# Performance work log

Measured on AMD Instinct MI355X. Metric: run time of the kernel, lower is better.

The kernel has to match this reference:

```python
import jax, jax.numpy as jnp
import numpy as np

K = 8               # top-k frequencies
PRED_LEN = 96       # prediction_length
LOW_FREQ = 1        # low_frequency cutoff (drops DC)


def setup_inputs() -> dict:
    key = jax.random.key(0)
    x = jax.random.normal(key, (32, 2048, 64), dtype=jnp.float32)
    return {"x": x}


def reference(x):
    b, t, d = x.shape
    x_freq = jnp.fft.rfft(x, axis=1)                 # (b, t//2+1, d) complex
    freqs = jnp.fft.rfftfreq(t).astype(x.dtype)
    if t % 2 == 0:
        x_freq = x_freq[:, LOW_FREQ:-1]              # drop DC and Nyquist
        f = freqs[LOW_FREQ:-1]
    else:
        x_freq = x_freq[:, LOW_FREQ:]
        f = freqs[LOW_FREQ:]

    # top-k over frequency dim (axis=1), independently per (b, d)
    mag = jnp.abs(x_freq)                            # (b, F, d)
    _, idx = jax.lax.top_k(jnp.moveaxis(mag, 1, 2), K)  # (b, d, K), sorted desc
    idx = jnp.moveaxis(idx, 1, 2)                    # (b, K, d)
    x_k = jnp.take_along_axis(x_freq, idx, axis=1)   # (b, K, d) complex
    f_k = f[idx]                                     # (b, K, d)

    # extrapolate: add conjugate (negative) frequencies, then cos-sum
    x2 = jnp.concatenate([x_k, jnp.conj(x_k)], axis=1)  # (b, 2K, d)
    f2 = jnp.concatenate([f_k, -f_k], axis=1)           # (b, 2K, d)
    t_val = jnp.arange(t + PRED_LEN, dtype=x.dtype)     # (T,)
    amp = jnp.abs(x2) / t                               # (b, 2K, d)
    phase = jnp.angle(x2)                               # (b, 2K, d)
    # (b, 2K, T, d) broadcast intermediate, reduced over freq axis
    x_time = amp[:, :, None, :] * jnp.cos(
        2.0 * np.float32(np.pi) * f2[:, :, None, :] * t_val[None, None, :, None]
        + phase[:, :, None, :]
    )
    return x_time.sum(axis=1)                        # (b, t+PRED_LEN, d)
```

## Files before the change

### kernel.cpp

```cpp
#include <hip/hip_runtime.h>
#include <math.h>

#define BB 32
#define TT 2048
#define DD 64
#define PRED 96
#define TP (TT + PRED)
#define KTOP 8
#define MARGIN 8e-4f
#define PI_D 3.14159265358979323846

__device__ __forceinline__ int br6(int l) { return (int)(__brev((unsigned)l) >> 26); }
static constexpr int BR5[32] = {0,16,8,24,4,20,12,28,2,18,10,26,6,22,14,30,
                                1,17,9,25,5,21,13,29,3,19,11,27,7,23,15,31};
static constexpr float C32T[16] = {
    1.0f, 0.98078528040323044913f, 0.92387953251128675613f, 0.83146961230254523708f,
    0.70710678118654752440f, 0.55557023301960222474f, 0.38268343236508977173f, 0.19509032201612826785f,
    0.0f, -0.19509032201612826785f, -0.38268343236508977173f, -0.55557023301960222474f,
    -0.70710678118654752440f, -0.83146961230254523708f, -0.92387953251128675613f, -0.98078528040323044913f};
static constexpr float S32T[16] = {
    0.0f, 0.19509032201612826785f, 0.38268343236508977173f, 0.55557023301960222474f,
    0.70710678118654752440f, 0.83146961230254523708f, 0.92387953251128675613f, 0.98078528040323044913f,
    1.0f, 0.98078528040323044913f, 0.92387953251128675613f, 0.83146961230254523708f,
    0.70710678118654752440f, 0.55557023301960222474f, 0.38268343236508977173f, 0.19509032201612826785f};

__device__ __forceinline__ float2 ctw(float2 a, int m) {
    const float rev = (float)m * (1.0f / 2048.0f);
    const float c = __builtin_amdgcn_cosf(rev);
    const float s = __builtin_amdgcn_sinf(rev);
    return make_float2(a.x * c + a.y * s, a.y * c - a.x * s);
}

__global__ __launch_bounds__(256) void fused_kernel(const float* __restrict__ x,
                                                    float* __restrict__ out) {
    __shared__ float SRe[4][2112];
    __shared__ float SIm[4][2112];
    __shared__ int   coefK[8][KTOP];
    __shared__ float coefR[8][KTOP], coefI[8][KTOP];

    const int t    = threadIdx.x;
    const int wv   = t >> 6, lane = t & 63;
    const int bid  = blockIdx.x;
    const int xcd  = bid & 7;
    const int idx  = bid >> 3;
    const int b    = xcd * 4 + (idx >> 3);
    const int grp  = idx & 7;
    const int dp   = grp * 4 + wv;
    const int d_base = grp * 8;

    const float2* xv = (const float2*)x;
    const size_t xbase = (size_t)b * TT * (DD / 2) + dp;

    float2 v[32];
    #pragma unroll
    for (int i = 0; i < 32; ++i)
        v[i] = xv[xbase + (size_t)(64 * BR5[i] + lane) * (DD / 2)];

    #pragma unroll
    for (int s = 1; s <= 5; ++s) {
        const int m = 1 << s, half = m >> 1, stepw = 32 >> s;
        #pragma unroll
        for (int g = 0; g < 32; g += m) {
            #pragma unroll
            for (int j = 0; j < half; ++j) {
                const float c = C32T[j * stepw], sn = S32T[j * stepw];
                const int i0 = g + j, i1 = i0 + half;
                const float tr = c * v[i1].x + sn * v[i1].y;
                const float ti = c * v[i1].y - sn * v[i1].x;
                v[i1] = make_float2(v[i0].x - tr, v[i0].y - ti);
                v[i0] = make_float2(v[i0].x + tr, v[i0].y + ti);
            }
        }
    }

    #pragma unroll
    for (int q = 1; q < 32; ++q) v[q] = ctw(v[q], (lane * q) & (TT - 1));

    {
        const int rl = br6(lane);
        #pragma unroll
        for (int q = 0; q < 32; ++q) {
            v[q].x = __shfl(v[q].x, rl, 64);
            v[q].y = __shfl(v[q].y, rl, 64);
        }
    }
    #pragma unroll
    for (int s = 1; s <= 6; ++s) {
        const int half = 1 << (s - 1);
        const float rev = (float)(lane & (half - 1)) / (float)(1 << s);
        const float wc  = __builtin_amdgcn_cosf(rev);
        const float wsn = __builtin_amdgcn_sinf(rev);
        const bool  hi  = (lane & half) != 0;
        #pragma unroll
        for (int q = 0; q < 32; ++q) {
            float2 pv;
            pv.x = __shfl_xor(v[q].x, half, 64);
            pv.y = __shfl_xor(v[q].y, half, 64);
            const float2 bsv = hi ? v[q] : pv;
            const float2 asv = hi ? pv : v[q];
            const float tr = wc * bsv.x + wsn * bsv.y;
            const float ti = wc * bsv.y - wsn * bsv.x;
            v[q] = hi ? make_float2(asv.x - tr, asv.y - ti)
                      : make_float2(asv.x + tr, asv.y + ti);
        }
    }

    #pragma unroll
    for (int q = 0; q < 32; ++q) {
        const int a = 33 * lane + q;
        SRe[wv][a] = v[q].x;
        SIm[wv][a] = v[q].y;
    }
    __syncthreads();

    const int sig = lane >> 5, hl = lane & 31;
    unsigned A[32];
    #pragma unroll
    for (int q = 0; q < 32; ++q) {
        const int k = 32 * hl + q;
        unsigned kk = 0u;
        if (k != 0) {
            const int a1 = k + (k >> 5);
            const int pk = TT - k, a2 = pk + (pk >> 5);
            const float zr = SRe[wv][a1], zi = SIm[wv][a1];
            const float yr = SRe[wv][a2], yi = SIm[wv][a2];
            float cr, ci;
            if (sig == 0) { cr = 0.5f * (zr + yr); ci = 0.5f * (zi - yi); }
            else          { cr = 0.5f * (zi + yi); ci = 0.5f * (yr - zr); }
            const float mg = cr * cr + ci * ci;
            kk = (__float_as_uint(mg) & 0xFFFFF800u) | (unsigned)(2047 - k);
        }
        A[q] = kk;
    }

    #pragma unroll
    for (int sz = 2; sz <= 32; sz <<= 1) {
        #pragma unroll
        for (int d = sz >> 1; d > 0; d >>= 1) {
            #pragma unroll
            for (int i2 = 0; i2 < 32; ++i2) {
                const int j2i = i2 ^ d;
                if (j2i > i2) {
                    const bool desc = ((i2 & sz) == 0);
                    const unsigned a = A[i2], b2 = A[j2i];
                    const unsigned mx = a > b2 ? a : b2, mn = a > b2 ? b2 : a;
                    A[i2] = desc ? mx : mn;  A[j2i] = desc ? mn : mx;
                }
            }
        }
    }
    #pragma unroll
    for (int off = 1; off <= 16; off <<= 1) {
        unsigned Bv[32];
        #pragma unroll
        for (int i2 = 0; i2 < 32; ++i2)
            Bv[i2] = (unsigned)__shfl_xor((int)A[i2], off, 64);
        #pragma unroll
        for (int i2 = 0; i2 < 32; ++i2) {
            const unsigned o = Bv[31 - i2];
            A[i2] = A[i2] > o ? A[i2] : o;
        }
        #pragma unroll
        for (int d = 16; d > 0; d >>= 1) {
            #pragma unroll
            for (int i2 = 0; i2 < 32; ++i2) {
                if ((i2 & d) == 0) {
                    const int j2i = i2 + d;
                    const unsigned a = A[i2], b2 = A[j2i];
                    A[i2] = a > b2 ? a : b2;  A[j2i] = a > b2 ? b2 : a;
                }
            }
        }
    }

    const float m8f = __uint_as_float(A[7] & 0xFFFFF800u);
    unsigned bandmask = 0u;
    #pragma unroll
    for (int r = 0; r < 16; ++r) {
        const float mr = __uint_as_float(A[r] & 0xFFFFF800u);
        if (fabsf(mr - m8f) <= MARGIN * m8f) bandmask |= (1u << r);
    }
    const int flg = (bandmask != (1u << 7)) ? 1 : 0;

    unsigned myk = 0u;
    #pragma unroll
    for (int i2 = 0; i2 < 16; ++i2) myk = (hl == i2) ? A[i2] : myk;
    const int kcand = 2047 - (int)(myk & 0x7FFu);
    const int s_local = 2 * wv + sig;

    if (!flg && hl < KTOP) {
        const int k = kcand, a1 = k + (k >> 5), pk = TT - k, a2 = pk + (pk >> 5);
        const float zr = SRe[wv][a1], zi = SIm[wv][a1];
        const float yr = SRe[wv][a2], yi = SIm[wv][a2];
        float cr, ci;
        if (sig == 0) { cr = 0.5f * (zr + yr); ci = 0.5f * (zi - yi); }
        else          { cr = 0.5f * (zi + yi); ci = 0.5f * (yr - zr); }
        coefK[s_local][hl] = k;
        coefR[s_local][hl] = cr * (2.0f / (float)TT);
        coefI[s_local][hl] = ci * (2.0f / (float)TT);
    }

    const int flg0 = __shfl(flg, 0, 64);
    const int flg1 = __shfl(flg, 32, 64);

    if (flg0 | flg1) {
        float2 sv[32];
        #pragma unroll
        for (int m = 0; m < 32; ++m)
            sv[m] = xv[xbase + (size_t)(lane + 64 * m) * (DD / 2)];
        const double thA = -2.0 * PI_D * (double)lane / 64.0;
        const double thB = -2.0 * PI_D * (double)lane / (double)TT;
        const double wac = cos(thA), was = sin(thA);
        const double wbc = cos(thB), wbs = sin(thB);

        for (int sg = 0; sg < 2; ++sg) {
            const int flg_s = (sg == 0) ? flg0 : flg1;
            if (!flg_s) continue;
            const unsigned bm = (unsigned)__shfl((int)bandmask, 32 * sg, 64);
            const int lo = (int)__builtin_ctz(bm);
            double myM = 0.0, myR = 0.0, myI = 0.0;
            for (int r = 0; r < 16; ++r) {
                if (!((bm >> r) & 1u)) continue;
                const int kr = __shfl(kcand, 32 * sg + r, 64);
                double ar = 0.0, ai = 0.0;
                for (int m = 0; m < 32; ++m) {
                    const int n  = lane + 64 * m;
                    const int mm = (n * kr) & (TT - 1);
                    const double qc  = __shfl(wac, mm >> 5, 64);
                    const double qs  = __shfl(was, mm >> 5, 64);
                    const double rc2 = __shfl(wbc, mm & 31, 64);
                    const double rs2 = __shfl(wbs, mm & 31, 64);
                    const double wr = qc * rc2 - qs * rs2;
                    const double wi = qc * rs2 + qs * rc2;
                    const double xs = (sg == 0) ? (double)sv[m].x : (double)sv[m].y;
                    ar = fma(xs, wr, ar);
                    ai = fma(xs, wi, ai);
                }
                #pragma unroll
                for (int off = 32; off; off >>= 1) {
                    ar += __shfl_xor(ar, off, 64);
                    ai += __shfl_xor(ai, off, 64);
                }
                if (lane == 32 * sg + r) { myM = ar * ar + ai * ai; myR = ar; myI = ai; }
            }
            const int h16 = hl & 15;
            const double selfM = __shfl(myM, 32 * sg + h16, 64);
            const int    selfK = __shfl(kcand, 32 * sg + h16, 64);
            int rb = 0;
            for (int r2 = 0; r2 < 16; ++r2) {
                if (!((bm >> r2) & 1u)) continue;
                const double om = __shfl(myM, 32 * sg + r2, 64);
                const int    ok = __shfl(kcand, 32 * sg + r2, 64);
                if (r2 != h16 && (om > selfM || (om == selfM && ok < selfK))) ++rb;
            }
            const int isband = (int)((bm >> h16) & 1u);
            const int rank = isband ? (lo + rb) : h16;
            if (sig == sg && hl < 16 && rank < KTOP) {
                coefK[s_local][rank] = kcand;
                if (isband) {
                    coefR[s_local][rank] = (float)(myR * (2.0 / (double)TT));
                    coefI[s_local][rank] = (float)(myI * (2.0 / (double)TT));
                } else {
                    const int k = kcand, a1 = k + (k >> 5), pk = TT - k, a2 = pk + (pk >> 5);
                    const float zr = SRe[wv][a1], zi = SIm[wv][a1];
                    const float yr = SRe[wv][a2], yi = SIm[wv][a2];
                    float cr, ci;
                    if (sg == 0) { cr = 0.5f * (zr + yr); ci = 0.5f * (zi - yi); }
                    else          { cr = 0.5f * (zi + yi); ci = 0.5f * (yr - zr); }
                    coefR[s_local][rank] = cr * (2.0f / (float)TT);
                    coefI[s_local][rank] = ci * (2.0f / (float)TT);
                }
            }
        }
    }
    __syncthreads();

    const int d8 = t & 7, tq = t >> 3;
    int   kc[KTOP];
    float fr[KTOP], fi[KTOP], pc[KTOP], ps[KTOP], rc[KTOP], rs[KTOP];
    #pragma unroll
    for (int p = 0; p < KTOP; ++p) {
        kc[p] = coefK[d8][p];
        fr[p] = coefR[d8][p];
        fi[p] = coefI[d8][p];
        const int j0 = (kc[p] * tq) & (TT - 1);
        const float rv0 = (float)j0 * (1.0f / 2048.0f);
        pc[p] = __builtin_amdgcn_cosf(rv0);
        ps[p] = __builtin_amdgcn_sinf(rv0);
        const int jr = (kc[p] * 32) & (TT - 1);
        const float rvr = (float)jr * (1.0f / 2048.0f);
        rc[p] = __builtin_amdgcn_cosf(rvr);
        rs[p] = __builtin_amdgcn_sinf(rvr);
    }
    float* op = out + (size_t)b * TP * DD + d_base + d8;
    #pragma unroll 4
    for (int m = 0; m < 67; ++m) {
        const int tv = tq + 32 * m;
        float acc = 0.0f;
        #pragma unroll
        for (int p = 0; p < KTOP; ++p) acc += fr[p] * pc[p] - fi[p] * ps[p];
        op[(size_t)tv * DD] = acc;
        #pragma unroll
        for (int p = 0; p < KTOP; ++p) {
            const float nc = pc[p] * rc[p] - ps[p] * rs[p];
            const float ns = pc[p] * rs[p] + ps[p] * rc[p];
            pc[p] = nc; ps[p] = ns;
        }
    }
}

extern "C" void kernel_launch(void* const* d_in, const int* in_sizes, int n_in,
                              void* d_out, int out_size, void* d_ws, size_t ws_size,
                              hipStream_t stream) {
    const float* x = (const float*)d_in[0];
    float* out = (float*)d_out;
    (void)d_ws; (void)ws_size; (void)in_sizes; (void)n_in; (void)out_size;

    fused_kernel<<<BB * 8, 256, 0, stream>>>(x, out);
}
```

Measured before the change: 112.6 us.

## Stage output through reused LDS pool, trim top-k merge, drop redundant barrier

Merges the FFT scratch arrays into one shared pool. After the coefficient barrier, that pool is reused as an output tile, and the tile is written back to global memory in a flat thread-indexed loop. The cross-lane top-k merge now keeps only the top 16 candidates instead of 32, which cuts shuffles and compare-swaps. The barrier after the per-wave FFT store is removed because each wave reads only its own slice. The staged write still emits 8-float row segments at stride 64, much like before, so it adds LDS traffic and a barrier for little coalescing gain.

```diff
diff --git a/kernel.cpp b/kernel.cpp
--- a/kernel.cpp
+++ b/kernel.cpp
@@ -31,10 +31,13 @@
     return make_float2(a.x * c + a.y * s, a.y * c - a.x * s);
 }
 
+#define SRE(w,a) POOL[(w) * 2112 + (a)]
+#define SIM(w,a) POOL[8448 + (w) * 2112 + (a)]
+#define TILE(tv,d8) POOL[(tv) * 8 + (d8)]
+
 __global__ __launch_bounds__(256) void fused_kernel(const float* __restrict__ x,
                                                     float* __restrict__ out) {
-    __shared__ float SRe[4][2112];
-    __shared__ float SIm[4][2112];
+    __shared__ float POOL[17152];
     __shared__ int   coefK[8][KTOP];
     __shared__ float coefR[8][KTOP], coefI[8][KTOP];
 
@@ -108,10 +111,9 @@
     #pragma unroll
     for (int q = 0; q < 32; ++q) {
         const int a = 33 * lane + q;
-        SRe[wv][a] = v[q].x;
-        SIm[wv][a] = v[q].y;
-    }
-    __syncthreads();
+        SRE(wv, a) = v[q].x;
+        SIM(wv, a) = v[q].y;
+    }
 
     const int sig = lane >> 5, hl = lane & 31;
     unsigned A[32];
@@ -122,8 +124,8 @@
         if (k != 0) {
             const int a1 = k + (k >> 5);
             const int pk = TT - k, a2 = pk + (pk >> 5);
-            const float zr = SRe[wv][a1], zi = SIm[wv][a1];
-            const float yr = SRe[wv][a2], yi = SIm[wv][a2];
+            const float zr = SRE(wv, a1), zi = SIM(wv, a1);
+            const float yr = SRE(wv, a2), yi = SIM(wv, a2);
             float cr, ci;
             if (sig == 0) { cr = 0.5f * (zr + yr); ci = 0.5f * (zi - yi); }
             else          { cr = 0.5f * (zi + yi); ci = 0.5f * (yr - zr); }
@@ -151,19 +153,19 @@
     }
     #pragma unroll
     for (int off = 1; off <= 16; off <<= 1) {
-        unsigned Bv[32];
-        #pragma unroll
-        for (int i2 = 0; i2 < 32; ++i2)
+        unsigned Bv[16];
+        #pragma unroll
+        for (int i2 = 0; i2 < 16; ++i2)
             Bv[i2] = (unsigned)__shfl_xor((int)A[i2], off, 64);
         #pragma unroll
-        for (int i2 = 0; i2 < 32; ++i2) {
-            const unsigned o = Bv[31 - i2];
+        for (int i2 = 0; i2 < 16; ++i2) {
+            const unsigned o = Bv[15 - i2];
             A[i2] = A[i2] > o ? A[i2] : o;
         }
         #pragma unroll
-        for (int d = 16; d > 0; d >>= 1) {
+        for (int d = 8; d > 0; d >>= 1) {
             #pragma unroll
-            for (int i2 = 0; i2 < 32; ++i2) {
+            for (int i2 = 0; i2 < 16; ++i2) {
                 if ((i2 & d) == 0) {
                     const int j2i = i2 + d;
                     const unsigned a = A[i2], b2 = A[j2i];
@@ -190,8 +192,8 @@
 
     if (!flg && hl < KTOP) {
         const int k = kcand, a1 = k + (k >> 5), pk = TT - k, a2 = pk + (pk >> 5);
-        const float zr = SRe[wv][a1], zi = SIm[wv][a1];
-        const float yr = SRe[wv][a2], yi = SIm[wv][a2];
+        const float zr = SRE(wv, a1), zi = SIM(wv, a1);
+        const float yr = SRE(wv, a2), yi = SIM(wv, a2);
         float cr, ci;
         if (sig == 0) { cr = 0.5f * (zr + yr); ci = 0.5f * (zi - yi); }
         else          { cr = 0.5f * (zi + yi); ci = 0.5f * (yr - zr); }
@@ -262,8 +264,8 @@
                     coefI[s_local][rank] = (float)(myI * (2.0 / (double)TT));
                 } else {
                     const int k = kcand, a1 = k + (k >> 5), pk = TT - k, a2 = pk + (pk >> 5);
-                    const float zr = SRe[wv][a1], zi = SIm[wv][a1];
-                    const float yr = SRe[wv][a2], yi = SIm[wv][a2];
+                    const float zr = SRE(wv, a1), zi = SIM(wv, a1);
+                    const float yr = SRE(wv, a2), yi = SIM(wv, a2);
                     float cr, ci;
                     if (sg == 0) { cr = 0.5f * (zr + yr); ci = 0.5f * (zi - yi); }
                     else          { cr = 0.5f * (zi + yi); ci = 0.5f * (yr - zr); }
@@ -292,20 +294,27 @@
         rc[p] = __builtin_amdgcn_cosf(rvr);
         rs[p] = __builtin_amdgcn_sinf(rvr);
     }
-    float* op = out + (size_t)b * TP * DD + d_base + d8;
     #pragma unroll 4
     for (int m = 0; m < 67; ++m) {
         const int tv = tq + 32 * m;
         float acc = 0.0f;
         #pragma unroll
         for (int p = 0; p < KTOP; ++p) acc += fr[p] * pc[p] - fi[p] * ps[p];
-        op[(size_t)tv * DD] = acc;
+        TILE(tv, d8) = acc;
         #pragma unroll
         for (int p = 0; p < KTOP; ++p) {
             const float nc = pc[p] * rc[p] - ps[p] * rs[p];
             const float ns = pc[p] * rs[p] + ps[p] * rc[p];
             pc[p] = nc; ps[p] = ns;
         }
+    }
+    __syncthreads();
+
+    float* ob = out + (size_t)b * TP * DD + d_base;
+    for (int it = 0; it < 67; ++it) {
+        const int f  = it * 256 + t;
+        const int dd = f & 7, tv = f >> 3;
+        ob[(size_t)tv * DD + dd] = POOL[f];
     }
 }
 
```

Measured after the change: 110.9 us. No clear change (-1.5%).
